# Optimization experiments

Measured on AMD Instinct MI355X. Metric: run time of the kernel, lower is better.

Reference implementation:

```python
import jax, jax.numpy as jnp
import numpy as np

B, N, C = 32, 2048, 3
K = 20
E = 64  # embed_dim
BN_EPS = 1e-5


def setup_inputs() -> dict:
    key = jax.random.key(0)
    k1, k2, k3, k4 = jax.random.split(key, 4)
    xyz = jax.random.normal(k1, (B, N, C), dtype=jnp.float32)
    # Conv2d(6, E, kernel_size=1, bias=False) -> weight [E, 6]
    W = jax.random.normal(k2, (E, 2 * C), dtype=jnp.float32) * (1.0 / np.sqrt(2 * C))
    gamma = jnp.ones((E,), dtype=jnp.float32)
    beta = jnp.zeros((E,), dtype=jnp.float32)
    return {"xyz": xyz, "W": W, "gamma": gamma, "beta": beta}


def _forward(xyz, W, gamma, beta):
    # --- KNN: idx of k largest of negative squared distance ---
    dot = jnp.einsum("bnc,bmc->bnm", xyz, xyz)            # [B,N,N]
    xx = jnp.sum(xyz * xyz, axis=-1)                       # [B,N]
    pdist = 2.0 * dot - xx[:, :, None] - xx[:, None, :]    # -||xi-xj||^2
    idx = jax.lax.top_k(pdist, K)[1]                        # [B,N,K] int32
    # --- gather neighbors (index_points) ---
    grouped = jax.vmap(lambda pts, i: pts[i])(xyz, idx)    # [B,N,K,C]
    xyz_rep = jnp.broadcast_to(xyz[:, :, None, :], (B, N, K, C))
    edge = jnp.concatenate([xyz_rep, grouped - xyz_rep], axis=-1)  # [B,N,K,2C]
    # --- 1x1 conv (pointwise matmul) ---
    h = jnp.einsum("bnkc,ec->bnke", edge, W)               # [B,N,K,E]
    # --- BatchNorm2d (training-mode batch stats over B,N,K per channel) ---
    mean = jnp.mean(h, axis=(0, 1, 2))
    var = jnp.mean(jnp.square(h - mean), axis=(0, 1, 2))   # biased var
    hn = (h - mean) * jax.lax.rsqrt(var + BN_EPS) * gamma + beta
    # --- hardswish: x * relu6(x + 3) / 6 ---
    a = hn * jnp.clip(hn + 3.0, 0.0, 6.0) * (1.0 / 6.0)
    # --- max over k neighbors, output [B,E,N] ---
    x = jnp.max(a, axis=2)                                  # [B,N,E]
    return xyz, jnp.transpose(x, (0, 2, 1))                 # [B,E,N]


def reference(xyz, W, gamma, beta):
    return _forward(xyz, W, gamma, beta)
```

## Files before the change

kernel.cpp:

```cpp
#include <hip/hip_runtime.h>
#include <math.h>

#define Bdim 32
#define Ndim 2048
#define Cdim 3
#define Kdim 20
#define Edim 64
#define NPART 27
#define NBLK1 2048
#define CNT (Bdim * Ndim * Kdim)

#define NEG_INF __int_as_float(0xFF800000)

#define DPPU(v, ctrl) \
  ((unsigned)__builtin_amdgcn_update_dpp((int)(v), (int)(v), (ctrl), 0xf, 0xf, false))
#define DPPF(v, ctrl) \
  (__int_as_float(__builtin_amdgcn_update_dpp(__float_as_int(v), __float_as_int(v), (ctrl), 0xf, 0xf, false)))

__device__ __forceinline__ unsigned red_max_u32_l63(unsigned v) {
  unsigned t;
  t = DPPU(v, 0x121); v = (v > t) ? v : t;
  t = DPPU(v, 0x122); v = (v > t) ? v : t;
  t = DPPU(v, 0x124); v = (v > t) ? v : t;
  t = DPPU(v, 0x128); v = (v > t) ? v : t;
  t = DPPU(v, 0x142); v = (v > t) ? v : t;
  t = DPPU(v, 0x143); v = (v > t) ? v : t;
  return v;
}

__device__ __forceinline__ float red_max_f32_l63(float v) {
  float t;
  t = DPPF(v, 0x121); v = fmaxf(v, t);
  t = DPPF(v, 0x122); v = fmaxf(v, t);
  t = DPPF(v, 0x124); v = fmaxf(v, t);
  t = DPPF(v, 0x128); v = fmaxf(v, t);
  t = DPPF(v, 0x142); v = fmaxf(v, t);
  t = DPPF(v, 0x143); v = fmaxf(v, t);
  return v;
}

__device__ __forceinline__ float red_add_f32_l63(float v) {
  float t;
  t = DPPF(v, 0x121); v += t;
  t = DPPF(v, 0x122); v += t;
  t = DPPF(v, 0x124); v += t;
  t = DPPF(v, 0x128); v += t;
  t = DPPF(v, 0x142); v += t;
  t = DPPF(v, 0x143); v += t;
  return v;
}

__device__ __forceinline__ float sreadf(float v, int l) {
  return __int_as_float(__builtin_amdgcn_readlane(__float_as_int(v), l));
}

__global__ __launch_bounds__(512) void k1_knn_stats(
    const float* __restrict__ xyz, int* __restrict__ idx_out,
    float* __restrict__ partials) {
  __shared__ float4 pts[Ndim];
  __shared__ float red[8][NPART];

  const int b = blockIdx.y;
  const int tid = threadIdx.x;
  const float* xb = xyz + (size_t)b * Ndim * Cdim;

  float* sp = (float*)&pts[0];
  for (int g = tid; g < Ndim * Cdim; g += 512) {
    sp[(g / 3) * 4 + (g % 3)] = xb[g];
  }
  __syncthreads();
  for (int p = tid; p < Ndim; p += 512) {
    float4 q = pts[p];
    pts[p].w = q.x * q.x + q.y * q.y + q.z * q.z;
  }
  __syncthreads();

  const int w = tid >> 6;
  const int lane = tid & 63;

  float acc[NPART];
#pragma unroll
  for (int c = 0; c < NPART; ++c) acc[c] = 0.0f;

  for (int s = 0; s < 4; ++s) {
    const int i = blockIdx.x * 32 + w * 4 + s;
    const float4 pi = pts[i];

    unsigned mask = 0u;
    float h1 = NEG_INF, h2 = NEG_INF, h3 = NEG_INF;
    unsigned l1 = 0u, l2 = 0u, l3 = 0u;

#pragma unroll 8
    for (int t = 0; t < 32; ++t) {
      const int j = t * 64 + lane;
      const float4 pj = pts[j];
      const float dot = pi.x * pj.x + pi.y * pj.y + pi.z * pj.z;
      const float pd = 2.0f * dot - pi.w - pj.w;
      const bool b1 = pd > h1;
      const bool b2 = pd > h2;
      const bool b3 = pd > h3;
      h3 = b3 ? (b2 ? h2 : pd) : h3;  l3 = b3 ? (b2 ? l2 : (unsigned)t) : l3;
      h2 = b2 ? (b1 ? h1 : pd) : h2;  l2 = b2 ? (b1 ? l1 : (unsigned)t) : l2;
      h1 = b1 ? pd : h1;              l1 = b1 ? (unsigned)t : l1;
    }

    unsigned myJ = 0u;
    for (int r = 0; r < Kdim; ++r) {
      const float bm = red_max_f32_l63(h1);
      const float bestk = sreadf(bm, 63);

      unsigned cand = (h1 == bestk) ? (2047u - (l1 * 64u + (unsigned)lane)) : 0u;
      cand = red_max_u32_l63(cand);
      const unsigned jwin =
          2047u - (unsigned)__builtin_amdgcn_readlane((int)cand, 63);
      myJ = ((unsigned)lane == (unsigned)r) ? jwin : myJ;

      const bool win = ((unsigned)lane == (jwin & 63u));
      const bool pop = win && (h2 != NEG_INF);
      const bool resc = win && (h2 == NEG_INF);
      mask |= win ? (1u << (jwin >> 6)) : 0u;
      h1 = pop ? h2 : h1;  l1 = pop ? l2 : l1;
      h2 = pop ? h3 : h2;  l2 = pop ? l3 : l2;
      h3 = pop ? NEG_INF : h3;
      if (resc) {
        float a1 = NEG_INF, a2 = NEG_INF, a3 = NEG_INF;
        unsigned c1 = 0u, c2 = 0u, c3 = 0u;
        for (int t = 0; t < 32; ++t) {
          if (mask & (1u << t)) continue;
          const int j = t * 64 + lane;
          const float4 pj = pts[j];
          const float dot = pi.x * pj.x + pi.y * pj.y + pi.z * pj.z;
          const float pd = 2.0f * dot - pi.w - pj.w;
          const bool b1 = pd > a1;
          const bool b2 = pd > a2;
          const bool b3 = pd > a3;
          a3 = b3 ? (b2 ? a2 : pd) : a3;  c3 = b3 ? (b2 ? c2 : (unsigned)t) : c3;
          a2 = b2 ? (b1 ? a1 : pd) : a2;  c2 = b2 ? (b1 ? c1 : (unsigned)t) : c2;
          a1 = b1 ? pd : a1;              c1 = b1 ? (unsigned)t : c1;
        }
        h1 = a1; l1 = c1; h2 = a2; l2 = c2; h3 = a3; l3 = c3;
      }
    }

    if (lane < Kdim) {
      idx_out[((size_t)b * Ndim + i) * Kdim + lane] = (int)myJ;
      const float4 pj = pts[myJ];
      float ev[6];
      ev[0] = pi.x; ev[1] = pi.y; ev[2] = pi.z;
      ev[3] = pj.x - pi.x; ev[4] = pj.y - pi.y; ev[5] = pj.z - pi.z;
#pragma unroll
      for (int a = 0; a < 6; ++a) acc[a] += ev[a];
      int c = 6;
#pragma unroll
      for (int a = 0; a < 6; ++a)
#pragma unroll
        for (int d = a; d < 6; ++d) { acc[c] += ev[a] * ev[d]; ++c; }
    }
  }

#pragma unroll
  for (int c = 0; c < NPART; ++c) {
    const float v = red_add_f32_l63(acc[c]);
    if (lane == 63) red[w][c] = v;
  }
  __syncthreads();
  if (tid < NPART) {
    const int bid = blockIdx.y * gridDim.x + blockIdx.x;
    float v = 0.0f;
#pragma unroll
    for (int q = 0; q < 8; ++q) v += red[q][tid];
    partials[(size_t)bid * NPART + tid] = v;
  }
}

__global__ __launch_bounds__(256) void k2_bnstats(
    const float* __restrict__ partials, const float* __restrict__ W,
    const float* __restrict__ gamma, const float* __restrict__ beta,
    float* __restrict__ ss) {
  __shared__ double stat[NPART];
  __shared__ double red[4];
  const int tid = threadIdx.x;
  const int lane = tid & 63;
  const int w = tid >> 6;

  for (int c = 0; c < NPART; ++c) {
    double v = 0.0;
    for (int p = tid; p < NBLK1; p += 256) v += (double)partials[(size_t)p * NPART + c];
#pragma unroll
    for (int d = 1; d < 64; d <<= 1) v += __shfl_xor(v, d, 64);
    if (lane == 0) red[w] = v;
    __syncthreads();
    if (tid == 0) stat[c] = red[0] + red[1] + red[2] + red[3];
    __syncthreads();
  }

  if (tid < Edim) {
    const double inv = 1.0 / (double)CNT;
    double mu[6];
#pragma unroll
    for (int c = 0; c < 6; ++c) mu[c] = stat[c] * inv;
    double wv[6];
#pragma unroll
    for (int c = 0; c < 6; ++c) wv[c] = (double)W[tid * 6 + c];
    double m = 0.0;
#pragma unroll
    for (int c = 0; c < 6; ++c) m += wv[c] * mu[c];
    double q = 0.0;
    int s = 6;
#pragma unroll
    for (int a = 0; a < 6; ++a)
#pragma unroll
      for (int d = a; d < 6; ++d) {
        q += (a == d ? 1.0 : 2.0) * wv[a] * wv[d] * (stat[s] * inv);
        ++s;
      }
    const double var = q - m * m;
    const double rstd = 1.0 / sqrt(var + 1e-5);
    const float scale = (float)((double)gamma[tid] * rstd);
    const float shift = (float)((double)beta[tid] - m * rstd * (double)gamma[tid]);
    ss[tid] = scale;
    ss[Edim + tid] = shift;
  }
}

__global__ __launch_bounds__(512) void k3_out(
    const float* __restrict__ xyz, const int* __restrict__ idx,
    const float* __restrict__ W, const float* __restrict__ ss,
    float* __restrict__ out) {
  __shared__ float4 pts[Ndim];
  __shared__ float sm[128][65];
  const int b = blockIdx.y;
  const int n0 = blockIdx.x * 128;
  const int tid = threadIdx.x;
  const int w = tid >> 6;
  const int lane = tid & 63;
  const float* xb = xyz + (size_t)b * Ndim * Cdim;

  float* sp = (float*)&pts[0];
  for (int g = tid; g < Ndim * Cdim; g += 512) {
    sp[(g / 3) * 4 + (g % 3)] = xb[g];
  }
  __syncthreads();

  float wv[6];
#pragma unroll
  for (int c = 0; c < 6; ++c) wv[c] = W[lane * 6 + c];
  const float scale = ss[lane];
  const float shift = ss[Edim + lane];

  for (int s = 0; s < 16; ++s) {
    const int i = n0 + w * 16 + s;
    const float4 pi = pts[i];
    const float hbase = wv[0] * pi.x + wv[1] * pi.y + wv[2] * pi.z;
    const int* ip = idx + ((size_t)b * Ndim + i) * Kdim;
    float m = -INFINITY;
    for (int k = 0; k < Kdim; ++k) {
      const int j = __builtin_amdgcn_readfirstlane(ip[k]);
      const float4 pj = pts[j];
      const float h = hbase + wv[3] * (pj.x - pi.x) + wv[4] * (pj.y - pi.y) +
                      wv[5] * (pj.z - pi.z);
      const float a = h * scale + shift;
      const float r6 = fminf(fmaxf(a + 3.0f, 0.0f), 6.0f);
      const float hs = a * r6 * (1.0f / 6.0f);
      m = fmaxf(m, hs);
    }
    sm[w * 16 + s][lane] = m;
  }
  __syncthreads();

#pragma unroll
  for (int r = 0; r < 8; ++r) {
    const int e = r * 8 + w;
    out[((size_t)b * Edim + e) * Ndim + n0 + lane] = sm[lane][e];
    out[((size_t)b * Edim + e) * Ndim + n0 + 64 + lane] = sm[64 + lane][e];
  }
}

extern "C" void kernel_launch(void* const* d_in, const int* in_sizes, int n_in,
                              void* d_out, int out_size, void* d_ws, size_t ws_size,
                              hipStream_t stream) {
  const float* xyz = (const float*)d_in[0];
  const float* W = (const float*)d_in[1];
  const float* gamma = (const float*)d_in[2];
  const float* beta = (const float*)d_in[3];
  float* out = (float*)d_out;

  char* ws = (char*)d_ws;
  int* idx = (int*)ws;
  float* partials = (float*)(ws + (size_t)Bdim * Ndim * Kdim * 4);
  float* ss = (float*)(ws + (size_t)Bdim * Ndim * Kdim * 4 + (size_t)NBLK1 * NPART * 4);

  hipMemcpyAsync(out, xyz, (size_t)Bdim * Ndim * Cdim * sizeof(float),
                 hipMemcpyDeviceToDevice, stream);

  k1_knn_stats<<<dim3(Ndim / 32, Bdim), 512, 0, stream>>>(xyz, idx, partials);
  k2_bnstats<<<1, 256, 0, stream>>>(partials, W, gamma, beta, ss);
  k3_out<<<dim3(Ndim / 128, Bdim), 512, 0, stream>>>(
      xyz, idx, W, ss, out + (size_t)Bdim * Ndim * Cdim);
}
```

Measured before the change: 283.7 us.

## Split each wavefront into two half-waves to process two query points at once

The KNN kernel now lets each 32-lane half of a wavefront handle its own query point, so every wave does two queries per pass instead of one. Each lane keeps its top-3 over 64 candidates instead of 32, and the per-round reductions stop at 32 lanes, dropping one DPP step. A ballot fast path uses readlane to find the winning index when exactly one lane per half holds the max, falling back to the integer max-reduction when there are ties. This halves the serial top-K selection rounds per point. In exchange each lane's candidate scan is twice as long and rescans touch up to 64 slots.

New measurement: 340.9 us. 20.2% more time.

```diff
diff --git a/kernel.cpp b/kernel.cpp
--- a/kernel.cpp
+++ b/kernel.cpp
@@ -17,25 +17,23 @@
 #define DPPF(v, ctrl) \
   (__int_as_float(__builtin_amdgcn_update_dpp(__float_as_int(v), __float_as_int(v), (ctrl), 0xf, 0xf, false)))
 
-__device__ __forceinline__ unsigned red_max_u32_l63(unsigned v) {
+__device__ __forceinline__ float red_max_f32_halves(float v) {
+  float t;
+  t = DPPF(v, 0x121); v = fmaxf(v, t);
+  t = DPPF(v, 0x122); v = fmaxf(v, t);
+  t = DPPF(v, 0x124); v = fmaxf(v, t);
+  t = DPPF(v, 0x128); v = fmaxf(v, t);
+  t = DPPF(v, 0x142); v = fmaxf(v, t);
+  return v;
+}
+
+__device__ __forceinline__ unsigned red_max_u32_halves(unsigned v) {
   unsigned t;
   t = DPPU(v, 0x121); v = (v > t) ? v : t;
   t = DPPU(v, 0x122); v = (v > t) ? v : t;
   t = DPPU(v, 0x124); v = (v > t) ? v : t;
   t = DPPU(v, 0x128); v = (v > t) ? v : t;
   t = DPPU(v, 0x142); v = (v > t) ? v : t;
-  t = DPPU(v, 0x143); v = (v > t) ? v : t;
-  return v;
-}
-
-__device__ __forceinline__ float red_max_f32_l63(float v) {
-  float t;
-  t = DPPF(v, 0x121); v = fmaxf(v, t);
-  t = DPPF(v, 0x122); v = fmaxf(v, t);
-  t = DPPF(v, 0x124); v = fmaxf(v, t);
-  t = DPPF(v, 0x128); v = fmaxf(v, t);
-  t = DPPF(v, 0x142); v = fmaxf(v, t);
-  t = DPPF(v, 0x143); v = fmaxf(v, t);
   return v;
 }
 
@@ -77,22 +75,26 @@
 
   const int w = tid >> 6;
   const int lane = tid & 63;
+  const int half = lane >> 5;
+  const int hl = lane & 31;
 
   float acc[NPART];
 #pragma unroll
   for (int c = 0; c < NPART; ++c) acc[c] = 0.0f;
 
-  for (int s = 0; s < 4; ++s) {
-    const int i = blockIdx.x * 32 + w * 4 + s;
+  const int i0 = blockIdx.x * 32 + w * 4;
+
+  for (int q = 0; q < 2; ++q) {
+    const int i = i0 + 2 * q + half;
     const float4 pi = pts[i];
 
-    unsigned mask = 0u;
+    unsigned long long mask = 0ull;
     float h1 = NEG_INF, h2 = NEG_INF, h3 = NEG_INF;
     unsigned l1 = 0u, l2 = 0u, l3 = 0u;
 
 #pragma unroll 8
-    for (int t = 0; t < 32; ++t) {
-      const int j = t * 64 + lane;
+    for (int t = 0; t < 64; ++t) {
+      const int j = t * 32 + hl;
       const float4 pj = pts[j];
       const float dot = pi.x * pj.x + pi.y * pj.y + pi.z * pj.z;
       const float pd = 2.0f * dot - pi.w - pj.w;
@@ -106,28 +108,45 @@
 
     unsigned myJ = 0u;
     for (int r = 0; r < Kdim; ++r) {
-      const float bm = red_max_f32_l63(h1);
-      const float bestk = sreadf(bm, 63);
-
-      unsigned cand = (h1 == bestk) ? (2047u - (l1 * 64u + (unsigned)lane)) : 0u;
-      cand = red_max_u32_l63(cand);
-      const unsigned jwin =
-          2047u - (unsigned)__builtin_amdgcn_readlane((int)cand, 63);
-      myJ = ((unsigned)lane == (unsigned)r) ? jwin : myJ;
-
-      const bool win = ((unsigned)lane == (jwin & 63u));
+      const float bm = red_max_f32_halves(h1);
+      const float bkA = sreadf(bm, 31);
+      const float bkB = sreadf(bm, 63);
+      const float bestk = half ? bkB : bkA;
+
+      const unsigned long long mb = __ballot(h1 == bestk);
+      const unsigned lo = (unsigned)mb;
+      const unsigned hi = (unsigned)(mb >> 32);
+      unsigned jwinA, jwinB;
+      if (((lo & (lo - 1u)) | (hi & (hi - 1u))) == 0u) {
+        const int wlA = __ffs(lo) - 1;
+        const int wlB = 32 + __ffs(hi) - 1;
+        jwinA = ((unsigned)__builtin_amdgcn_readlane((int)l1, wlA)) * 32u +
+                (unsigned)wlA;
+        jwinB = ((unsigned)__builtin_amdgcn_readlane((int)l1, wlB)) * 32u +
+                ((unsigned)wlB & 31u);
+      } else {
+        unsigned cand =
+            (h1 == bestk) ? (2047u - (l1 * 32u + (unsigned)hl)) : 0u;
+        cand = red_max_u32_halves(cand);
+        jwinA = 2047u - (unsigned)__builtin_amdgcn_readlane((int)cand, 31);
+        jwinB = 2047u - (unsigned)__builtin_amdgcn_readlane((int)cand, 63);
+      }
+      const unsigned jwin = half ? jwinB : jwinA;
+      myJ = ((unsigned)hl == (unsigned)r) ? jwin : myJ;
+
+      const bool win = ((unsigned)hl == (jwin & 31u));
       const bool pop = win && (h2 != NEG_INF);
       const bool resc = win && (h2 == NEG_INF);
-      mask |= win ? (1u << (jwin >> 6)) : 0u;
+      mask |= win ? (1ull << (jwin >> 5)) : 0ull;
       h1 = pop ? h2 : h1;  l1 = pop ? l2 : l1;
       h2 = pop ? h3 : h2;  l2 = pop ? l3 : l2;
       h3 = pop ? NEG_INF : h3;
       if (resc) {
         float a1 = NEG_INF, a2 = NEG_INF, a3 = NEG_INF;
         unsigned c1 = 0u, c2 = 0u, c3 = 0u;
-        for (int t = 0; t < 32; ++t) {
-          if (mask & (1u << t)) continue;
-          const int j = t * 64 + lane;
+        for (int t = 0; t < 64; ++t) {
+          if (mask & (1ull << t)) continue;
+          const int j = t * 32 + hl;
           const float4 pj = pts[j];
           const float dot = pi.x * pj.x + pi.y * pj.y + pi.z * pj.z;
           const float pd = 2.0f * dot - pi.w - pj.w;
@@ -142,8 +161,8 @@
       }
     }
 
-    if (lane < Kdim) {
-      idx_out[((size_t)b * Ndim + i) * Kdim + lane] = (int)myJ;
+    if (hl < Kdim) {
+      idx_out[((size_t)b * Ndim + i) * Kdim + hl] = (int)myJ;
       const float4 pj = pts[myJ];
       float ev[6];
       ev[0] = pi.x; ev[1] = pi.y; ev[2] = pi.z;
@@ -168,7 +187,7 @@
     const int bid = blockIdx.y * gridDim.x + blockIdx.x;
     float v = 0.0f;
 #pragma unroll
-    for (int q = 0; q < 8; ++q) v += red[q][tid];
+    for (int qq = 0; qq < 8; ++qq) v += red[qq][tid];
     partials[(size_t)bid * NPART + tid] = v;
   }
 }
```
